# Kernel optimization log

Hardware: AMD Instinct MI355X
Metric: run time of the kernel (lower is better)

## Reference

```python
import jax, jax.numpy as jnp
import numpy as np

N_NODES = 100000
N_EDGES = 1600000
IN_FT = 128
OUT_FT = 32


def setup_inputs() -> dict:
    key = jax.random.key(0)
    k_seq, k_w, k_row, k_col, k_val = jax.random.split(key, 5)
    seq = jax.random.normal(k_seq, (N_NODES, IN_FT), dtype=jnp.float32)
    # xavier_uniform with gain=1.414 for weight [in_ft, out_ft]
    limit = 1.414 * np.sqrt(6.0 / (IN_FT + OUT_FT))
    weight = jax.random.uniform(k_w, (IN_FT, OUT_FT), dtype=jnp.float32,
                                minval=-limit, maxval=limit)
    edge_row = jax.random.randint(k_row, (N_EDGES,), 0, N_NODES, dtype=jnp.int64)
    edge_col = jax.random.randint(k_col, (N_EDGES,), 0, N_NODES, dtype=jnp.int64)
    edge_val = jax.random.uniform(k_val, (N_EDGES,), dtype=jnp.float32)
    return {"seq": seq, "weight": weight, "edge_row": edge_row,
            "edge_col": edge_col, "edge_val": edge_val}


def reference(seq, weight, edge_row, edge_col, edge_val):
    # support = seq @ weight : dense projection [N, out_ft]
    support = seq @ weight
    # out = spmm(adj, support): adj in COO (row, col, val), out[i] = sum_e val_e * support[col_e]
    msgs = edge_val[:, None] * support[edge_col]          # [E, out_ft]
    out = jax.ops.segment_sum(msgs, edge_row, num_segments=N_NODES)
    return jax.nn.relu(out)
```

## Files before the change

### kernel.cpp

```cpp
#include <hip/hip_runtime.h>
#include <hip/hip_bf16.h>
#include <hip/hip_fp16.h>

#define IN_FT  128
#define OUT_FT 32
#define APITCH 136

#define RPB   256
#define CAP   8192
#define ACC_T 1024
#define BIN_E 4096

typedef _Float16 f16x8 __attribute__((ext_vector_type(8)));
typedef __attribute__((ext_vector_type(4))) float f32x4;

union H2 { unsigned u; _Float16 h[2]; };

__global__ __launch_bounds__(256) void gcn_swz(const float* __restrict__ w,
                                               _Float16* __restrict__ wtab) {
    int t = threadIdx.x;
    for (int i = t; i < 2 * 4 * 64 * 8; i += 256) {
        int j    = i & 7;
        int lane = (i >> 3) & 63;
        int kt   = (i >> 9) & 3;
        int tile = i >> 11;
        int k    = kt * 32 + (lane >> 4) * 8 + j;
        int c    = (lane & 15) + tile * 16;
        wtab[i] = (_Float16)w[k * OUT_FT + c];
    }
}

__global__ __launch_bounds__(256) void gcn_gemm_bin(const float* __restrict__ seq,
                                                    const _Float16* __restrict__ wtab,
                                                    unsigned short* __restrict__ sup,
                                                    const int* __restrict__ erow,
                                                    const int* __restrict__ ecol,
                                                    const float* __restrict__ eval,
                                                    int* __restrict__ bptr,
                                                    uint2* __restrict__ ebin,
                                                    int n, int nE, int gb) {
    __shared__ __align__(16) _Float16 at[64 * APITCH];
    const int t = threadIdx.x;

    if ((int)blockIdx.x >= gb) {
        int* cnt = (int*)at;
        int* cur = cnt + 512;
        cnt[t] = 0;
        cnt[t + 256] = 0;
        __syncthreads();

        const int cb = ((int)blockIdx.x - gb) * BIN_E;
        const int ce = min(cb + BIN_E, nE);

        #pragma unroll
        for (int k = 0; k < 4; ++k) {
            int i0 = cb + (k * 256 + t) * 4;
            if (i0 + 4 <= ce) {
                int4 r4 = *(const int4*)&erow[i0];
                atomicAdd(&cnt[r4.x >> 8], 1);
                atomicAdd(&cnt[r4.y >> 8], 1);
                atomicAdd(&cnt[r4.z >> 8], 1);
                atomicAdd(&cnt[r4.w >> 8], 1);
            } else {
                for (int i = i0; i < ce; ++i)
                    atomicAdd(&cnt[erow[i] >> 8], 1);
            }
        }
        __syncthreads();

        if (cnt[t])       cur[t]       = atomicAdd(&bptr[t],       cnt[t]);
        if (cnt[t + 256]) cur[t + 256] = atomicAdd(&bptr[t + 256], cnt[t + 256]);
        __syncthreads();

        #pragma unroll
        for (int k = 0; k < 4; ++k) {
            int i0 = cb + (k * 256 + t) * 4;
            if (i0 + 4 <= ce) {
                int4   r4 = *(const int4*)&erow[i0];
                int4   c4 = *(const int4*)&ecol[i0];
                float4 v4 = *(const float4*)&eval[i0];
                int      rr[4] = {r4.x, r4.y, r4.z, r4.w};
                unsigned cq[4];
                cq[0] = ((unsigned)c4.x << 15) | (unsigned)(v4.x * 32767.f + 0.5f);
                cq[1] = ((unsigned)c4.y << 15) | (unsigned)(v4.y * 32767.f + 0.5f);
                cq[2] = ((unsigned)c4.z << 15) | (unsigned)(v4.z * 32767.f + 0.5f);
                cq[3] = ((unsigned)c4.w << 15) | (unsigned)(v4.w * 32767.f + 0.5f);
                #pragma unroll
                for (int q = 0; q < 4; ++q) {
                    int b = rr[q] >> 8;
                    int p = atomicAdd(&cur[b], 1);
                    if (p < CAP) {
                        uint2 e;
                        e.x = cq[q];
                        e.y = (unsigned)(rr[q] & 255);
                        ebin[(size_t)b * CAP + p] = e;
                    }
                }
            } else {
                for (int i = i0; i < ce; ++i) {
                    int      r = erow[i];
                    unsigned q = ((unsigned)ecol[i] << 15)
                               | (unsigned)(eval[i] * 32767.f + 0.5f);
                    int b = r >> 8;
                    int p = atomicAdd(&cur[b], 1);
                    if (p < CAP) {
                        uint2 e;
                        e.x = q;
                        e.y = (unsigned)(r & 255);
                        ebin[(size_t)b * CAP + p] = e;
                    }
                }
            }
        }
        return;
    }

    const int base = blockIdx.x * 64;

    for (int it = 0; it < 4; ++it) {
        int i     = it * 256 + t;
        int row_l = i >> 4;
        int c     = i & 15;
        int row   = base + row_l;
        f16x8 v = (f16x8)0;
        if (row < n) {
            const float4* p = (const float4*)(seq + (size_t)row * IN_FT + c * 8);
            float4 lo = p[0], hi = p[1];
            v[0] = (_Float16)lo.x; v[1] = (_Float16)lo.y;
            v[2] = (_Float16)lo.z; v[3] = (_Float16)lo.w;
            v[4] = (_Float16)hi.x; v[5] = (_Float16)hi.y;
            v[6] = (_Float16)hi.z; v[7] = (_Float16)hi.w;
        }
        *(f16x8*)&at[row_l * APITCH + c * 8] = v;
    }
    __syncthreads();

    const int wave = t >> 6;
    const int lane = t & 63;
    const int m    = lane & 15;
    const int quad = lane >> 4;

    const f16x8* wt = (const f16x8*)wtab;
    const int arow_l = wave * 16 + m;

    f32x4 acc0 = {0.f, 0.f, 0.f, 0.f};
    f32x4 acc1 = {0.f, 0.f, 0.f, 0.f};

    for (int kt = 0; kt < 4; ++kt) {
        f16x8 a  = *(const f16x8*)&at[arow_l * APITCH + kt * 32 + quad * 8];
        f16x8 b0 = wt[(0 * 4 + kt) * 64 + lane];
        f16x8 b1 = wt[(1 * 4 + kt) * 64 + lane];
        acc0 = __builtin_amdgcn_mfma_f32_16x16x32_f16(a, b0, acc0, 0, 0, 0);
        acc1 = __builtin_amdgcn_mfma_f32_16x16x32_f16(a, b1, acc1, 0, 0, 0);
    }

    for (int i = 0; i < 4; ++i) {
        int ro = base + wave * 16 + quad * 4 + i;
        if (ro < n) {
            _Float16 h0 = (_Float16)acc0[i];
            _Float16 h1 = (_Float16)acc1[i];
            sup[(size_t)ro * OUT_FT + m]      = *(unsigned short*)&h0;
            sup[(size_t)ro * OUT_FT + 16 + m] = *(unsigned short*)&h1;
        }
    }
}

__global__ __launch_bounds__(ACC_T) void gcn_acc(const uint2* __restrict__ ebin,
                                                 const int* __restrict__ bptr,
                                                 const unsigned* __restrict__ sup32,
                                                 float2* __restrict__ out, int n) {
    __shared__ unsigned csr[CAP];
    __shared__ int hist[RPB];
    __shared__ int segs[RPB];
    __shared__ int cursor[RPB];
    const int    t    = threadIdx.x;
    const int    b    = blockIdx.x;
    const int    cnt  = min(bptr[b], CAP);
    const size_t base = (size_t)b * CAP;

    if (t < RPB) hist[t] = 0;
    __syncthreads();

    for (int i = t; i < cnt; i += ACC_T)
        atomicAdd(&hist[ebin[base + i].y], 1);
    __syncthreads();

    int v = 0;
    if (t < RPB) { v = hist[t]; segs[t] = v; }
    __syncthreads();
    for (int o = 1; o < RPB; o <<= 1) {
        int x = 0;
        if (t < RPB && t >= o) x = segs[t - o];
        __syncthreads();
        if (t < RPB) segs[t] += x;
        __syncthreads();
    }
    if (t < RPB) cursor[t] = segs[t] - v;
    __syncthreads();

    for (int i = t; i < cnt; i += ACC_T) {
        uint2 e = ebin[base + i];
        int   p = atomicAdd(&cursor[e.y], 1);
        csr[p] = e.x;
    }
    __syncthreads();

    const int g = t >> 4;
    const int j = t & 15;
    const int rbase = b * RPB;
    for (int rr = g; rr < RPB; rr += ACC_T / 16) {
        int end = segs[rr];
        int st  = end - hist[rr];
        float a0 = 0.f, a1 = 0.f;
        int e = st;
        for (; e + 2 <= end; e += 2) {
            unsigned c0 = csr[e], c1 = csr[e + 1];
            H2 s0; s0.u = sup32[(c0 >> 15) * 16 + j];
            H2 s1; s1.u = sup32[(c1 >> 15) * 16 + j];
            float v0 = (float)(c0 & 0x7fffu) * (1.f / 32767.f);
            float v1 = (float)(c1 & 0x7fffu) * (1.f / 32767.f);
            a0 += v0 * (float)s0.h[0] + v1 * (float)s1.h[0];
            a1 += v0 * (float)s0.h[1] + v1 * (float)s1.h[1];
        }
        if (e < end) {
            unsigned c0 = csr[e];
            H2 s0; s0.u = sup32[(c0 >> 15) * 16 + j];
            float v0 = (float)(c0 & 0x7fffu) * (1.f / 32767.f);
            a0 += v0 * (float)s0.h[0];
            a1 += v0 * (float)s0.h[1];
        }
        int row = rbase + rr;
        if (row < n) {
            float2 o;
            o.x = fmaxf(a0, 0.f);
            o.y = fmaxf(a1, 0.f);
            out[(size_t)row * 16 + j] = o;
        }
    }
}

extern "C" void kernel_launch(void* const* d_in, const int* in_sizes, int n_in,
                              void* d_out, int out_size, void* d_ws, size_t ws_size,
                              hipStream_t stream) {
    const float* seq  = (const float*)d_in[0];
    const float* w    = (const float*)d_in[1];
    const int*   erow = (const int*)d_in[2];
    const int*   ecol = (const int*)d_in[3];
    const float* eval = (const float*)d_in[4];
    float* out = (float*)d_out;

    const int n_nodes = in_sizes[0] / IN_FT;
    const int n_edges = in_sizes[2];
    const int nB      = (n_nodes + RPB - 1) / RPB;

    unsigned short* sup  = (unsigned short*)d_ws;
    uint2*          ebin = (uint2*)(sup + (size_t)n_nodes * OUT_FT);
    int*            bptr = (int*)(ebin + (size_t)nB * CAP);
    _Float16*       wtab = (_Float16*)(bptr + 512);

    hipMemsetAsync(bptr, 0, 512 * sizeof(int), stream);

    gcn_swz<<<1, 256, 0, stream>>>(w, wtab);

    int gb = (n_nodes + 63) / 64;
    int bb = (n_edges + BIN_E - 1) / BIN_E;
    gcn_gemm_bin<<<gb + bb, 256, 0, stream>>>(seq, wtab, sup, erow, ecol, eval,
                                              bptr, ebin, n_nodes, n_edges, gb);

    gcn_acc<<<nB, ACC_T, 0, stream>>>(ebin, bptr, (const unsigned*)sup,
                                      (float2*)out, n_nodes);
}
```

Measured before the change: 162.5 us.

## Split edge bins into packed arrays and precompute per-row counts globally

Edge bins are now stored as a 4-byte column/value array plus a 1-byte local-row array instead of 8-byte pairs, which cuts bin write and read traffic. Per-row histograms are built with global atomics during binning, so the accumulate kernel no longer makes its own histogram pass over the bin. The separate memset is folded into the weight-swizzle kernel, which now also clears the row counters. The trade-off is 1.6M extra global atomics in the binning phase, plus bounds clamps added for overflowing bins.

```diff
diff --git a/kernel.cpp b/kernel.cpp
--- a/kernel.cpp
+++ b/kernel.cpp
@@ -17,16 +17,24 @@
 union H2 { unsigned u; _Float16 h[2]; };
 
 __global__ __launch_bounds__(256) void gcn_swz(const float* __restrict__ w,
-                                               _Float16* __restrict__ wtab) {
-    int t = threadIdx.x;
-    for (int i = t; i < 2 * 4 * 64 * 8; i += 256) {
-        int j    = i & 7;
-        int lane = (i >> 3) & 63;
-        int kt   = (i >> 9) & 3;
-        int tile = i >> 11;
-        int k    = kt * 32 + (lane >> 4) * 8 + j;
-        int c    = (lane & 15) + tile * 16;
-        wtab[i] = (_Float16)w[k * OUT_FT + c];
+                                               _Float16* __restrict__ wtab,
+                                               int* __restrict__ bptr,
+                                               int* __restrict__ rs, int nR) {
+    int g = blockIdx.x * 256 + threadIdx.x;
+    for (int i = g; i < nR; i += gridDim.x * 256) rs[i] = 0;
+    if (blockIdx.x == 0) {
+        int t = threadIdx.x;
+        bptr[t] = 0;
+        bptr[t + 256] = 0;
+        for (int i = t; i < 2 * 4 * 64 * 8; i += 256) {
+            int j    = i & 7;
+            int lane = (i >> 3) & 63;
+            int kt   = (i >> 9) & 3;
+            int tile = i >> 11;
+            int k    = kt * 32 + (lane >> 4) * 8 + j;
+            int c    = (lane & 15) + tile * 16;
+            wtab[i] = (_Float16)w[k * OUT_FT + c];
+        }
     }
 }
 
@@ -37,7 +45,9 @@
                                                     const int* __restrict__ ecol,
                                                     const float* __restrict__ eval,
                                                     int* __restrict__ bptr,
-                                                    uint2* __restrict__ ebin,
+                                                    int* __restrict__ rs,
+                                                    unsigned* __restrict__ ecv,
+                                                    unsigned char* __restrict__ ery,
                                                     int n, int nE, int gb) {
     __shared__ __align__(16) _Float16 at[64 * APITCH];
     const int t = threadIdx.x;
@@ -61,9 +71,16 @@
                 atomicAdd(&cnt[r4.y >> 8], 1);
                 atomicAdd(&cnt[r4.z >> 8], 1);
                 atomicAdd(&cnt[r4.w >> 8], 1);
+                atomicAdd(&rs[r4.x], 1);
+                atomicAdd(&rs[r4.y], 1);
+                atomicAdd(&rs[r4.z], 1);
+                atomicAdd(&rs[r4.w], 1);
             } else {
-                for (int i = i0; i < ce; ++i)
-                    atomicAdd(&cnt[erow[i] >> 8], 1);
+                for (int i = i0; i < ce; ++i) {
+                    int r = erow[i];
+                    atomicAdd(&cnt[r >> 8], 1);
+                    atomicAdd(&rs[r], 1);
+                }
             }
         }
         __syncthreads();
@@ -90,10 +107,8 @@
                     int b = rr[q] >> 8;
                     int p = atomicAdd(&cur[b], 1);
                     if (p < CAP) {
-                        uint2 e;
-                        e.x = cq[q];
-                        e.y = (unsigned)(rr[q] & 255);
-                        ebin[(size_t)b * CAP + p] = e;
+                        ecv[(size_t)b * CAP + p] = cq[q];
+                        ery[(size_t)b * CAP + p] = (unsigned char)(rr[q] & 255);
                     }
                 }
             } else {
@@ -104,10 +119,8 @@
                     int b = r >> 8;
                     int p = atomicAdd(&cur[b], 1);
                     if (p < CAP) {
-                        uint2 e;
-                        e.x = q;
-                        e.y = (unsigned)(r & 255);
-                        ebin[(size_t)b * CAP + p] = e;
+                        ecv[(size_t)b * CAP + p] = q;
+                        ery[(size_t)b * CAP + p] = (unsigned char)(r & 255);
                     }
                 }
             }
@@ -165,8 +178,10 @@
     }
 }
 
-__global__ __launch_bounds__(ACC_T) void gcn_acc(const uint2* __restrict__ ebin,
+__global__ __launch_bounds__(ACC_T) void gcn_acc(const unsigned* __restrict__ ecv,
+                                                 const unsigned char* __restrict__ ery,
                                                  const int* __restrict__ bptr,
+                                                 const int* __restrict__ rs,
                                                  const unsigned* __restrict__ sup32,
                                                  float2* __restrict__ out, int n) {
     __shared__ unsigned csr[CAP];
@@ -178,16 +193,10 @@
     const int    cnt  = min(bptr[b], CAP);
     const size_t base = (size_t)b * CAP;
 
-    if (t < RPB) hist[t] = 0;
-    __syncthreads();
-
-    for (int i = t; i < cnt; i += ACC_T)
-        atomicAdd(&hist[ebin[base + i].y], 1);
-    __syncthreads();
-
     int v = 0;
-    if (t < RPB) { v = hist[t]; segs[t] = v; }
-    __syncthreads();
+    if (t < RPB) { v = rs[b * RPB + t]; hist[t] = v; segs[t] = v; }
+    __syncthreads();
+
     for (int o = 1; o < RPB; o <<= 1) {
         int x = 0;
         if (t < RPB && t >= o) x = segs[t - o];
@@ -198,10 +207,20 @@
     if (t < RPB) cursor[t] = segs[t] - v;
     __syncthreads();
 
-    for (int i = t; i < cnt; i += ACC_T) {
-        uint2 e = ebin[base + i];
-        int   p = atomicAdd(&cursor[e.y], 1);
-        csr[p] = e.x;
+    for (int i0 = t * 4; i0 < cnt; i0 += ACC_T * 4) {
+        if (i0 + 4 <= cnt) {
+            uchar4 ry = *(const uchar4*)&ery[base + i0];
+            uint4  cv = *(const uint4*) &ecv[base + i0];
+            int p0 = atomicAdd(&cursor[ry.x], 1); if (p0 < CAP) csr[p0] = cv.x;
+            int p1 = atomicAdd(&cursor[ry.y], 1); if (p1 < CAP) csr[p1] = cv.y;
+            int p2 = atomicAdd(&cursor[ry.z], 1); if (p2 < CAP) csr[p2] = cv.z;
+            int p3 = atomicAdd(&cursor[ry.w], 1); if (p3 < CAP) csr[p3] = cv.w;
+        } else {
+            for (int i = i0; i < cnt; ++i) {
+                int p = atomicAdd(&cursor[ery[base + i]], 1);
+                if (p < CAP) csr[p] = ecv[base + i];
+            }
+        }
     }
     __syncthreads();
 
@@ -209,8 +228,8 @@
     const int j = t & 15;
     const int rbase = b * RPB;
     for (int rr = g; rr < RPB; rr += ACC_T / 16) {
-        int end = segs[rr];
-        int st  = end - hist[rr];
+        int end = min(segs[rr], CAP);
+        int st  = max(end - hist[rr], 0);
         float a0 = 0.f, a1 = 0.f;
         int e = st;
         for (; e + 2 <= end; e += 2) {
@@ -252,21 +271,23 @@
     const int n_nodes = in_sizes[0] / IN_FT;
     const int n_edges = in_sizes[2];
     const int nB      = (n_nodes + RPB - 1) / RPB;
+    const int nR      = nB * RPB;
 
     unsigned short* sup  = (unsigned short*)d_ws;
-    uint2*          ebin = (uint2*)(sup + (size_t)n_nodes * OUT_FT);
-    int*            bptr = (int*)(ebin + (size_t)nB * CAP);
+    unsigned*       ecv  = (unsigned*)(sup + (size_t)n_nodes * OUT_FT);
+    unsigned char*  ery  = (unsigned char*)(ecv + (size_t)nB * CAP);
+    int*            rs   = (int*)(ery + (size_t)nB * CAP);
+    int*            bptr = rs + nR;
     _Float16*       wtab = (_Float16*)(bptr + 512);
 
-    hipMemsetAsync(bptr, 0, 512 * sizeof(int), stream);
-
-    gcn_swz<<<1, 256, 0, stream>>>(w, wtab);
+    gcn_swz<<<98, 256, 0, stream>>>(w, wtab, bptr, rs, nR);
 
     int gb = (n_nodes + 63) / 64;
     int bb = (n_edges + BIN_E - 1) / BIN_E;
     gcn_gemm_bin<<<gb + bb, 256, 0, stream>>>(seq, wtab, sup, erow, ecol, eval,
-                                              bptr, ebin, n_nodes, n_edges, gb);
-
-    gcn_acc<<<nB, ACC_T, 0, stream>>>(ebin, bptr, (const unsigned*)sup,
+                                              bptr, rs, ecv, ery,
+                                              n_nodes, n_edges, gb);
+
+    gcn_acc<<<nB, ACC_T, 0, stream>>>(ecv, ery, bptr, rs, (const unsigned*)sup,
                                       (float2*)out, n_nodes);
 }
```

New measurement: 213.8 us. 31.5% more time.
